# Performance work log

Hardware: AMD Instinct MI355X
Metric: run time of the kernel (lower is better)

The kernel has to match this reference:

```python
import jax, jax.numpy as jnp
import numpy as np
from jax import lax

WIN = 9
PAD = WIN // 2


def _box_sum(x):
    # x: [B,1,H,W]; all-ones WINxWIN conv, stride 1, pad PAD -> same spatial size
    k = jnp.ones((1, 1, WIN, WIN), dtype=x.dtype)
    return lax.conv_general_dilated(
        x, k, window_strides=(1, 1), padding=[(PAD, PAD), (PAD, PAD)],
        dimension_numbers=("NCHW", "OIHW", "NCHW"))


def setup_inputs() -> dict:
    key = jax.random.key(0)
    k1, k2 = jax.random.split(key)
    B, C, H, W = 32, 1, 512, 512
    y_true = jax.random.uniform(k1, (B, C, H, W), dtype=jnp.float32)
    y_pred = jax.random.uniform(k2, (B, C, H, W), dtype=jnp.float32)
    return {"y_true": y_true, "y_pred": y_pred}


def reference(y_true, y_pred):
    Ii, Ji = y_true, y_pred
    win_size = float(WIN * WIN)
    I_sum = _box_sum(Ii)
    J_sum = _box_sum(Ji)
    I2_sum = _box_sum(Ii * Ii)
    J2_sum = _box_sum(Ji * Ji)
    IJ_sum = _box_sum(Ii * Ji)
    u_I = I_sum / win_size
    u_J = J_sum / win_size
    cross = IJ_sum - u_J * I_sum - u_I * J_sum + u_I * u_J * win_size
    I_var = I2_sum - 2.0 * u_I * I_sum + u_I * u_I * win_size
    J_var = J2_sum - 2.0 * u_J * J_sum + u_J * u_J * win_size
    cc = cross * cross / (I_var * J_var + 1e-05)
    return -jnp.mean(cc)
```

## Files before the change

kernel.cpp:

```cpp
#include <hip/hip_runtime.h>


#define BATCH   32
#define IMH     512
#define IMW     512
#define SH      16
#define NSTRIP  32
#define NPART   (BATCH * NSTRIP)
#define VROW    520
#define NK      (SH + 8)

#define HWIN(QI, HA, HB) do {                                              \
    const float2 w0_ = *(const float2*)&Vbuf[QI][c0];                      \
    const float2 w1_ = *(const float2*)&Vbuf[QI][c0 + 2];                  \
    const float2 w2_ = *(const float2*)&Vbuf[QI][c0 + 4];                  \
    const float2 w3_ = *(const float2*)&Vbuf[QI][c0 + 6];                  \
    const float2 w4_ = *(const float2*)&Vbuf[QI][c0 + 8];                  \
    HA = ((w0_.x + w0_.y) + (w1_.x + w1_.y))                               \
       + ((w2_.x + w2_.y) + (w3_.x + w3_.y)) + w4_.x;                      \
    HB = HA + w4_.y - w0_.x;                                               \
} while (0)

#define CC1(AI, AJ, S2, S3, S4) do {                                       \
    const float cross = (S4) - (AI)*(AJ)*inv81;                            \
    const float ivv   = (S2) - (AI)*(AI)*inv81;                            \
    const float jvv   = (S3) - (AJ)*(AJ)*inv81;                            \
    acc += cross * cross * __builtin_amdgcn_rcpf(ivv * jvv + 1e-5f);       \
} while (0)

__global__ __launch_bounds__(256, 4) void ncc_main(const float* __restrict__ I,
                                                   const float* __restrict__ J,
                                                   float* __restrict__ partial) {
    const int u  = threadIdx.x;
    const int s  = blockIdx.x;
    const int b  = blockIdx.y;
    const int r0 = s * SH;
    const int c0 = 2 * u;
    const float inv81 = 1.0f / 81.0f;

    const float* Ib = I + (size_t)b * IMH * IMW;
    const float* Jb = J + (size_t)b * IMH * IMW;

    __shared__ float  Vbuf[5][VROW];
    __shared__ float4 ring[9][256];

    if (u < 40) {
        const int q = u >> 3, p = u & 7;
        Vbuf[q][p < 4 ? p : 512 + p] = 0.f;
    }
    __syncthreads();

    float VI0 = 0.f, VI1 = 0.f, VJ0 = 0.f, VJ1 = 0.f;
    float VII0 = 0.f, VII1 = 0.f, VJJ0 = 0.f, VJJ1 = 0.f;
    float VIJ0 = 0.f, VIJ1 = 0.f;
    float acc = 0.f;
    int slot = 0;

    float2 ai = make_float2(0.f, 0.f), aj = make_float2(0.f, 0.f);
    {
        const int ri = r0 - 4;
        if ((unsigned)ri < (unsigned)IMH) {
            ai = *(const float2*)(Ib + (size_t)ri * IMW + c0);
            aj = *(const float2*)(Jb + (size_t)ri * IMW + c0);
        }
    }

#pragma unroll 1
    for (int K = 0; K < NK; ++K) {
        float2 nai = make_float2(0.f, 0.f), naj = make_float2(0.f, 0.f);
        {
            const int rin = r0 - 3 + K;
            if (K + 1 < NK && (unsigned)rin < (unsigned)IMH) {
                nai = *(const float2*)(Ib + (size_t)rin * IMW + c0);
                naj = *(const float2*)(Jb + (size_t)rin * IMW + c0);
            }
        }

        float4 oldv = make_float4(0.f, 0.f, 0.f, 0.f);
        if (K >= 9) oldv = ring[slot][u];
        ring[slot][u] = make_float4(ai.x, ai.y, aj.x, aj.y);
        slot = (slot == 8) ? 0 : slot + 1;

        VI0  += ai.x - oldv.x;             VI1  += ai.y - oldv.y;
        VJ0  += aj.x - oldv.z;             VJ1  += aj.y - oldv.w;
        VII0 += ai.x*ai.x - oldv.x*oldv.x; VII1 += ai.y*ai.y - oldv.y*oldv.y;
        VJJ0 += aj.x*aj.x - oldv.z*oldv.z; VJJ1 += aj.y*aj.y - oldv.w*oldv.w;
        VIJ0 += ai.x*aj.x - oldv.x*oldv.z; VIJ1 += ai.y*aj.y - oldv.y*oldv.w;

        if (K >= 8) {
            *(float2*)&Vbuf[0][4 + c0] = make_float2(VI0,  VI1);
            *(float2*)&Vbuf[1][4 + c0] = make_float2(VJ0,  VJ1);
            *(float2*)&Vbuf[2][4 + c0] = make_float2(VII0, VII1);
            *(float2*)&Vbuf[3][4 + c0] = make_float2(VJJ0, VJJ1);
            *(float2*)&Vbuf[4][4 + c0] = make_float2(VIJ0, VIJ1);
            __syncthreads();
            float HI0, HI1, HJ0, HJ1, HA0, HA1, HB0, HB1, HC0, HC1;
            HWIN(0, HI0, HI1);
            HWIN(1, HJ0, HJ1);
            HWIN(2, HA0, HA1);
            HWIN(3, HB0, HB1);
            HWIN(4, HC0, HC1);
            CC1(HI0, HJ0, HA0, HB0, HC0);
            CC1(HI1, HJ1, HA1, HB1, HC1);
            __syncthreads();
        }

        ai = nai; aj = naj;
    }

    float sum = acc;
#pragma unroll
    for (int off = 32; off > 0; off >>= 1) sum += __shfl_down(sum, off, 64);

    __shared__ float wsum[4];
    if ((u & 63) == 0) wsum[u >> 6] = sum;
    __syncthreads();
    if (u == 0) {
        partial[(size_t)b * NSTRIP + s] = wsum[0] + wsum[1] + wsum[2] + wsum[3];
    }
}

__global__ __launch_bounds__(256) void ncc_reduce(const float* __restrict__ partial,
                                                  float* __restrict__ out) {
    const int t = threadIdx.x;
    double ssum = 0.0;
    for (int idx = t; idx < NPART; idx += 256) ssum += (double)partial[idx];
#pragma unroll
    for (int off = 32; off > 0; off >>= 1) ssum += __shfl_down(ssum, off, 64);

    __shared__ double wsum[4];
    if ((t & 63) == 0) wsum[t >> 6] = ssum;
    __syncthreads();
    if (t == 0) {
        const double total = wsum[0] + wsum[1] + wsum[2] + wsum[3];
        out[0] = (float)(-total / 8388608.0);
    }
}

extern "C" void kernel_launch(void* const* d_in, const int* in_sizes, int n_in,
                              void* d_out, int out_size, void* d_ws, size_t ws_size,
                              hipStream_t stream) {
    const float* I = (const float*)d_in[0];
    const float* J = (const float*)d_in[1];
    float* partial = (float*)d_ws;
    float* out     = (float*)d_out;

    dim3 grid(NSTRIP, BATCH);
    ncc_main<<<grid, 256, 0, stream>>>(I, J, partial);
    ncc_reduce<<<1, 256, 0, stream>>>(partial, out);
}
```

Measured before the change: 118.4 us.

## Split image rows into 128-column wavefront blocks with halo columns

Each 256-thread block handling a full 512-wide row strip is replaced by four 64-thread single-wavefront blocks, each covering 128 columns. Every block computes vertical sums for 8 extra halo columns, kept in a separate ring and written into a smaller shared buffer. The intent is cheaper barriers within one wavefront, a shorter cross-wave reduction, and more, smaller blocks for scheduling. In exchange, halo columns add redundant loads and vertical-sum work, and the halo loads and updates are done by only 8 lanes, which causes divergence.

```diff
diff --git a/kernel.cpp b/kernel.cpp
--- a/kernel.cpp
+++ b/kernel.cpp
@@ -1,21 +1,38 @@
 #include <hip/hip_runtime.h>
 
 
-#define BATCH   32
-#define IMH     512
-#define IMW     512
-#define SH      16
-#define NSTRIP  32
-#define NPART   (BATCH * NSTRIP)
-#define VROW    520
-#define NK      (SH + 8)
+#define BATCH     32
+#define IMH       512
+#define IMW       512
+#define SH        16
+#define NROWSTRIP 32
+#define NCOLSTRIP 4
+#define CBW       128
+#define NPART     (BATCH * NROWSTRIP * NCOLSTRIP)
+#define NK        (SH + 8)
+#define VROW      136
+
+#define LOADROW(RI, CI, CJ, HI, HJ) do {                                   \
+    const int ri_ = (RI);                                                  \
+    CI = make_float2(0.f, 0.f); CJ = make_float2(0.f, 0.f);                \
+    HI = 0.f; HJ = 0.f;                                                    \
+    if ((unsigned)ri_ < (unsigned)IMH) {                                   \
+        const float* rI_ = Ib + (size_t)ri_ * IMW;                         \
+        const float* rJ_ = Jb + (size_t)ri_ * IMW;                         \
+        CI = *(const float2*)(rI_ + cc0);                                  \
+        CJ = *(const float2*)(rJ_ + cc0);                                  \
+        if (u < 8 && (unsigned)hc < (unsigned)IMW) {                       \
+            HI = rI_[hc]; HJ = rJ_[hc];                                    \
+        }                                                                  \
+    }                                                                      \
+} while (0)
 
 #define HWIN(QI, HA, HB) do {                                              \
-    const float2 w0_ = *(const float2*)&Vbuf[QI][c0];                      \
-    const float2 w1_ = *(const float2*)&Vbuf[QI][c0 + 2];                  \
-    const float2 w2_ = *(const float2*)&Vbuf[QI][c0 + 4];                  \
-    const float2 w3_ = *(const float2*)&Vbuf[QI][c0 + 6];                  \
-    const float2 w4_ = *(const float2*)&Vbuf[QI][c0 + 8];                  \
+    const float2 w0_ = *(const float2*)&Vbuf[QI][l0];                      \
+    const float2 w1_ = *(const float2*)&Vbuf[QI][l0 + 2];                  \
+    const float2 w2_ = *(const float2*)&Vbuf[QI][l0 + 4];                  \
+    const float2 w3_ = *(const float2*)&Vbuf[QI][l0 + 6];                  \
+    const float2 w4_ = *(const float2*)&Vbuf[QI][l0 + 8];                  \
     HA = ((w0_.x + w0_.y) + (w1_.x + w1_.y))                               \
        + ((w2_.x + w2_.y) + (w3_.x + w3_.y)) + w4_.x;                      \
     HB = HA + w4_.y - w0_.x;                                               \
@@ -28,71 +45,73 @@
     acc += cross * cross * __builtin_amdgcn_rcpf(ivv * jvv + 1e-5f);       \
 } while (0)
 
-__global__ __launch_bounds__(256, 4) void ncc_main(const float* __restrict__ I,
-                                                   const float* __restrict__ J,
-                                                   float* __restrict__ partial) {
-    const int u  = threadIdx.x;
-    const int s  = blockIdx.x;
-    const int b  = blockIdx.y;
-    const int r0 = s * SH;
-    const int c0 = 2 * u;
+__global__ __launch_bounds__(64) void ncc_main(const float* __restrict__ I,
+                                               const float* __restrict__ J,
+                                               float* __restrict__ partial) {
+    const int u    = threadIdx.x;
+    const int cs   = blockIdx.x;
+    const int s    = blockIdx.y;
+    const int b    = blockIdx.z;
+    const int r0   = s * SH;
+    const int cblk = cs * CBW;
+    const int cc0  = cblk + 2 * u;
+    const int hc   = cblk + (u < 4 ? u - 4 : 124 + u);
+    const int hx   = (u < 4) ? u : 128 + u;
+    const int l0   = 2 * u;
     const float inv81 = 1.0f / 81.0f;
 
     const float* Ib = I + (size_t)b * IMH * IMW;
     const float* Jb = J + (size_t)b * IMH * IMW;
 
+    __shared__ float4 ring[9][64];
+    __shared__ float2 ringH[9][8];
     __shared__ float  Vbuf[5][VROW];
-    __shared__ float4 ring[9][256];
-
-    if (u < 40) {
-        const int q = u >> 3, p = u & 7;
-        Vbuf[q][p < 4 ? p : 512 + p] = 0.f;
-    }
-    __syncthreads();
 
     float VI0 = 0.f, VI1 = 0.f, VJ0 = 0.f, VJ1 = 0.f;
     float VII0 = 0.f, VII1 = 0.f, VJJ0 = 0.f, VJJ1 = 0.f;
     float VIJ0 = 0.f, VIJ1 = 0.f;
+    float hVI = 0.f, hVJ = 0.f, hVII = 0.f, hVJJ = 0.f, hVIJ = 0.f;
     float acc = 0.f;
     int slot = 0;
 
-    float2 ai = make_float2(0.f, 0.f), aj = make_float2(0.f, 0.f);
-    {
-        const int ri = r0 - 4;
-        if ((unsigned)ri < (unsigned)IMH) {
-            ai = *(const float2*)(Ib + (size_t)ri * IMW + c0);
-            aj = *(const float2*)(Jb + (size_t)ri * IMW + c0);
-        }
-    }
+    float2 ci, cj; float hi, hj;
+    LOADROW(r0 - 4, ci, cj, hi, hj);
 
 #pragma unroll 1
     for (int K = 0; K < NK; ++K) {
-        float2 nai = make_float2(0.f, 0.f), naj = make_float2(0.f, 0.f);
-        {
-            const int rin = r0 - 3 + K;
-            if (K + 1 < NK && (unsigned)rin < (unsigned)IMH) {
-                nai = *(const float2*)(Ib + (size_t)rin * IMW + c0);
-                naj = *(const float2*)(Jb + (size_t)rin * IMW + c0);
-            }
-        }
+        float2 ni, nj; float nhi, nhj;
+        LOADROW((K + 1 < NK) ? (r0 - 3 + K) : -1, ni, nj, nhi, nhj);
 
         float4 oldv = make_float4(0.f, 0.f, 0.f, 0.f);
-        if (K >= 9) oldv = ring[slot][u];
-        ring[slot][u] = make_float4(ai.x, ai.y, aj.x, aj.y);
+        float2 oldh = make_float2(0.f, 0.f);
+        if (K >= 9) {
+            oldv = ring[slot][u];
+            if (u < 8) oldh = ringH[slot][u];
+        }
+        ring[slot][u] = make_float4(ci.x, ci.y, cj.x, cj.y);
+        if (u < 8) ringH[slot][u] = make_float2(hi, hj);
         slot = (slot == 8) ? 0 : slot + 1;
 
-        VI0  += ai.x - oldv.x;             VI1  += ai.y - oldv.y;
-        VJ0  += aj.x - oldv.z;             VJ1  += aj.y - oldv.w;
-        VII0 += ai.x*ai.x - oldv.x*oldv.x; VII1 += ai.y*ai.y - oldv.y*oldv.y;
-        VJJ0 += aj.x*aj.x - oldv.z*oldv.z; VJJ1 += aj.y*aj.y - oldv.w*oldv.w;
-        VIJ0 += ai.x*aj.x - oldv.x*oldv.z; VIJ1 += ai.y*aj.y - oldv.y*oldv.w;
+        VI0  += ci.x - oldv.x;             VI1  += ci.y - oldv.y;
+        VJ0  += cj.x - oldv.z;             VJ1  += cj.y - oldv.w;
+        VII0 += ci.x*ci.x - oldv.x*oldv.x; VII1 += ci.y*ci.y - oldv.y*oldv.y;
+        VJJ0 += cj.x*cj.x - oldv.z*oldv.z; VJJ1 += cj.y*cj.y - oldv.w*oldv.w;
+        VIJ0 += ci.x*cj.x - oldv.x*oldv.z; VIJ1 += ci.y*cj.y - oldv.y*oldv.w;
+        hVI  += hi - oldh.x;               hVJ  += hj - oldh.y;
+        hVII += hi*hi - oldh.x*oldh.x;
+        hVJJ += hj*hj - oldh.y*oldh.y;
+        hVIJ += hi*hj - oldh.x*oldh.y;
 
         if (K >= 8) {
-            *(float2*)&Vbuf[0][4 + c0] = make_float2(VI0,  VI1);
-            *(float2*)&Vbuf[1][4 + c0] = make_float2(VJ0,  VJ1);
-            *(float2*)&Vbuf[2][4 + c0] = make_float2(VII0, VII1);
-            *(float2*)&Vbuf[3][4 + c0] = make_float2(VJJ0, VJJ1);
-            *(float2*)&Vbuf[4][4 + c0] = make_float2(VIJ0, VIJ1);
+            *(float2*)&Vbuf[0][4 + l0] = make_float2(VI0,  VI1);
+            *(float2*)&Vbuf[1][4 + l0] = make_float2(VJ0,  VJ1);
+            *(float2*)&Vbuf[2][4 + l0] = make_float2(VII0, VII1);
+            *(float2*)&Vbuf[3][4 + l0] = make_float2(VJJ0, VJJ1);
+            *(float2*)&Vbuf[4][4 + l0] = make_float2(VIJ0, VIJ1);
+            if (u < 8) {
+                Vbuf[0][hx] = hVI;  Vbuf[1][hx] = hVJ;  Vbuf[2][hx] = hVII;
+                Vbuf[3][hx] = hVJJ; Vbuf[4][hx] = hVIJ;
+            }
             __syncthreads();
             float HI0, HI1, HJ0, HJ1, HA0, HA1, HB0, HB1, HC0, HC1;
             HWIN(0, HI0, HI1);
@@ -105,18 +124,14 @@
             __syncthreads();
         }
 
-        ai = nai; aj = naj;
+        ci = ni; cj = nj; hi = nhi; hj = nhj;
     }
 
     float sum = acc;
 #pragma unroll
     for (int off = 32; off > 0; off >>= 1) sum += __shfl_down(sum, off, 64);
-
-    __shared__ float wsum[4];
-    if ((u & 63) == 0) wsum[u >> 6] = sum;
-    __syncthreads();
     if (u == 0) {
-        partial[(size_t)b * NSTRIP + s] = wsum[0] + wsum[1] + wsum[2] + wsum[3];
+        partial[((size_t)b * NROWSTRIP + s) * NCOLSTRIP + cs] = sum;
     }
 }
 
@@ -145,7 +160,7 @@
     float* partial = (float*)d_ws;
     float* out     = (float*)d_out;
 
-    dim3 grid(NSTRIP, BATCH);
-    ncc_main<<<grid, 256, 0, stream>>>(I, J, partial);
+    dim3 grid(NCOLSTRIP, NROWSTRIP, BATCH);
+    ncc_main<<<grid, 64, 0, stream>>>(I, J, partial);
     ncc_reduce<<<1, 256, 0, stream>>>(partial, out);
 }
```

Result: slower. 126.8 us (+7.0%).

## Fully unroll row loop with register ring buffer and 4-deep prefetch

Applied to the files above, without the earlier changes.

Replaces the shared-memory float4 ring buffer of the last 9 input rows with 18 named float2 registers. The row loop is fully unrolled so register indices are static, and global loads are now issued four rows ahead instead of one. This removes LDS traffic for the ring and hides more global-memory latency, at the cost of higher register pressure under launch_bounds(256,4) and larger code size.

```diff
diff --git a/kernel.cpp b/kernel.cpp
--- a/kernel.cpp
+++ b/kernel.cpp
@@ -7,8 +7,17 @@
 #define SH      16
 #define NSTRIP  32
 #define NPART   (BATCH * NSTRIP)
+#define NK      24
 #define VROW    520
-#define NK      (SH + 8)
+
+#define PREF(K, PI, PJ) do {                                               \
+    const int ri_ = r0 - 4 + (K);                                          \
+    PI = make_float2(0.f, 0.f); PJ = make_float2(0.f, 0.f);                \
+    if ((unsigned)ri_ < (unsigned)IMH) {                                   \
+        PI = *(const float2*)(Ib + (size_t)ri_ * IMW + c0);                \
+        PJ = *(const float2*)(Jb + (size_t)ri_ * IMW + c0);                \
+    }                                                                      \
+} while (0)
 
 #define HWIN(QI, HA, HB) do {                                              \
     const float2 w0_ = *(const float2*)&Vbuf[QI][c0];                      \
@@ -28,94 +37,110 @@
     acc += cross * cross * __builtin_amdgcn_rcpf(ivv * jvv + 1e-5f);       \
 } while (0)
 
+#define EMIT() do {                                                        \
+    *(float2*)&Vbuf[0][4 + c0] = make_float2(VI0, VI1);                    \
+    *(float2*)&Vbuf[1][4 + c0] = make_float2(VJ0, VJ1);                    \
+    *(float2*)&Vbuf[2][4 + c0] = make_float2(VA0, VA1);                    \
+    *(float2*)&Vbuf[3][4 + c0] = make_float2(VB0, VB1);                    \
+    *(float2*)&Vbuf[4][4 + c0] = make_float2(VC0, VC1);                    \
+    __syncthreads();                                                       \
+    float HI0, HI1, HJ0, HJ1, HA0, HA1, HB0, HB1, HC0, HC1;                \
+    HWIN(0, HI0, HI1);                                                     \
+    HWIN(1, HJ0, HJ1);                                                     \
+    HWIN(2, HA0, HA1);                                                     \
+    HWIN(3, HB0, HB1);                                                     \
+    HWIN(4, HC0, HC1);                                                     \
+    CC1(HI0, HJ0, HA0, HB0, HC0);                                          \
+    CC1(HI1, HJ1, HA1, HB1, HC1);                                          \
+    __syncthreads();           \
+} while (0)
+
+#define STEP(K, PI, PJ, RI_, RJ_) do {                                     \
+    if ((K) >= 9) {                                                        \
+        VI0 -= RI_.x;        VI1 -= RI_.y;                                 \
+        VJ0 -= RJ_.x;        VJ1 -= RJ_.y;                                 \
+        VA0 -= RI_.x*RI_.x;  VA1 -= RI_.y*RI_.y;                           \
+        VB0 -= RJ_.x*RJ_.x;  VB1 -= RJ_.y*RJ_.y;                           \
+        VC0 -= RI_.x*RJ_.x;  VC1 -= RI_.y*RJ_.y;                           \
+    }                                                                      \
+    VI0 += PI.x;        VI1 += PI.y;                                       \
+    VJ0 += PJ.x;        VJ1 += PJ.y;                                       \
+    VA0 += PI.x*PI.x;   VA1 += PI.y*PI.y;                                  \
+    VB0 += PJ.x*PJ.x;   VB1 += PJ.y*PJ.y;                                  \
+    VC0 += PI.x*PJ.x;   VC1 += PI.y*PJ.y;                                  \
+    RI_ = PI; RJ_ = PJ;                                                    \
+    if ((K) >= 8) { EMIT(); }                                              \
+} while (0)
+
 __global__ __launch_bounds__(256, 4) void ncc_main(const float* __restrict__ I,
                                                    const float* __restrict__ J,
                                                    float* __restrict__ partial) {
-    const int u  = threadIdx.x;
+    const int t  = threadIdx.x;
     const int s  = blockIdx.x;
     const int b  = blockIdx.y;
     const int r0 = s * SH;
-    const int c0 = 2 * u;
+    const int c0 = 2 * t;
     const float inv81 = 1.0f / 81.0f;
 
     const float* Ib = I + (size_t)b * IMH * IMW;
     const float* Jb = J + (size_t)b * IMH * IMW;
 
-    __shared__ float  Vbuf[5][VROW];
-    __shared__ float4 ring[9][256];
-
-    if (u < 40) {
-        const int q = u >> 3, p = u & 7;
+    __shared__ float Vbuf[5][VROW];
+    if (t < 40) {
+        const int q = t >> 3, p = t & 7;
         Vbuf[q][p < 4 ? p : 512 + p] = 0.f;
     }
     __syncthreads();
 
+    const float2 z_ = make_float2(0.f, 0.f);
+    float2 rIA = z_, rIB = z_, rIC = z_, rID = z_, rIE = z_,
+           rIF = z_, rIG = z_, rIH = z_, rII = z_;
+    float2 rJA = z_, rJB = z_, rJC = z_, rJD = z_, rJE = z_,
+           rJF = z_, rJG = z_, rJH = z_, rJI = z_;
     float VI0 = 0.f, VI1 = 0.f, VJ0 = 0.f, VJ1 = 0.f;
-    float VII0 = 0.f, VII1 = 0.f, VJJ0 = 0.f, VJJ1 = 0.f;
-    float VIJ0 = 0.f, VIJ1 = 0.f;
+    float VA0 = 0.f, VA1 = 0.f, VB0 = 0.f, VB1 = 0.f;
+    float VC0 = 0.f, VC1 = 0.f;
     float acc = 0.f;
-    int slot = 0;
+    float2 pi0, pj0, pi1, pj1, pi2, pj2, pi3, pj3;
 
-    float2 ai = make_float2(0.f, 0.f), aj = make_float2(0.f, 0.f);
-    {
-        const int ri = r0 - 4;
-        if ((unsigned)ri < (unsigned)IMH) {
-            ai = *(const float2*)(Ib + (size_t)ri * IMW + c0);
-            aj = *(const float2*)(Jb + (size_t)ri * IMW + c0);
-        }
-    }
+    PREF(0, pi0, pj0);
+    PREF(1, pi1, pj1);
+    PREF(2, pi2, pj2);
+    PREF(3, pi3, pj3);
 
-#pragma unroll 1
-    for (int K = 0; K < NK; ++K) {
-        float2 nai = make_float2(0.f, 0.f), naj = make_float2(0.f, 0.f);
-        {
-            const int rin = r0 - 3 + K;
-            if (K + 1 < NK && (unsigned)rin < (unsigned)IMH) {
-                nai = *(const float2*)(Ib + (size_t)rin * IMW + c0);
-                naj = *(const float2*)(Jb + (size_t)rin * IMW + c0);
-            }
-        }
-
-        float4 oldv = make_float4(0.f, 0.f, 0.f, 0.f);
-        if (K >= 9) oldv = ring[slot][u];
-        ring[slot][u] = make_float4(ai.x, ai.y, aj.x, aj.y);
-        slot = (slot == 8) ? 0 : slot + 1;
-
-        VI0  += ai.x - oldv.x;             VI1  += ai.y - oldv.y;
-        VJ0  += aj.x - oldv.z;             VJ1  += aj.y - oldv.w;
-        VII0 += ai.x*ai.x - oldv.x*oldv.x; VII1 += ai.y*ai.y - oldv.y*oldv.y;
-        VJJ0 += aj.x*aj.x - oldv.z*oldv.z; VJJ1 += aj.y*aj.y - oldv.w*oldv.w;
-        VIJ0 += ai.x*aj.x - oldv.x*oldv.z; VIJ1 += ai.y*aj.y - oldv.y*oldv.w;
-
-        if (K >= 8) {
-            *(float2*)&Vbuf[0][4 + c0] = make_float2(VI0,  VI1);
-            *(float2*)&Vbuf[1][4 + c0] = make_float2(VJ0,  VJ1);
-            *(float2*)&Vbuf[2][4 + c0] = make_float2(VII0, VII1);
-            *(float2*)&Vbuf[3][4 + c0] = make_float2(VJJ0, VJJ1);
-            *(float2*)&Vbuf[4][4 + c0] = make_float2(VIJ0, VIJ1);
-            __syncthreads();
-            float HI0, HI1, HJ0, HJ1, HA0, HA1, HB0, HB1, HC0, HC1;
-            HWIN(0, HI0, HI1);
-            HWIN(1, HJ0, HJ1);
-            HWIN(2, HA0, HA1);
-            HWIN(3, HB0, HB1);
-            HWIN(4, HC0, HC1);
-            CC1(HI0, HJ0, HA0, HB0, HC0);
-            CC1(HI1, HJ1, HA1, HB1, HC1);
-            __syncthreads();
-        }
-
-        ai = nai; aj = naj;
-    }
+    STEP( 0, pi0, pj0, rIA, rJA);  PREF( 4, pi0, pj0);
+    STEP( 1, pi1, pj1, rIB, rJB);  PREF( 5, pi1, pj1);
+    STEP( 2, pi2, pj2, rIC, rJC);  PREF( 6, pi2, pj2);
+    STEP( 3, pi3, pj3, rID, rJD);  PREF( 7, pi3, pj3);
+    STEP( 4, pi0, pj0, rIE, rJE);  PREF( 8, pi0, pj0);
+    STEP( 5, pi1, pj1, rIF, rJF);  PREF( 9, pi1, pj1);
+    STEP( 6, pi2, pj2, rIG, rJG);  PREF(10, pi2, pj2);
+    STEP( 7, pi3, pj3, rIH, rJH);  PREF(11, pi3, pj3);
+    STEP( 8, pi0, pj0, rII, rJI);  PREF(12, pi0, pj0);
+    STEP( 9, pi1, pj1, rIA, rJA);  PREF(13, pi1, pj1);
+    STEP(10, pi2, pj2, rIB, rJB);  PREF(14, pi2, pj2);
+    STEP(11, pi3, pj3, rIC, rJC);  PREF(15, pi3, pj3);
+    STEP(12, pi0, pj0, rID, rJD);  PREF(16, pi0, pj0);
+    STEP(13, pi1, pj1, rIE, rJE);  PREF(17, pi1, pj1);
+    STEP(14, pi2, pj2, rIF, rJF);  PREF(18, pi2, pj2);
+    STEP(15, pi3, pj3, rIG, rJG);  PREF(19, pi3, pj3);
+    STEP(16, pi0, pj0, rIH, rJH);  PREF(20, pi0, pj0);
+    STEP(17, pi1, pj1, rII, rJI);  PREF(21, pi1, pj1);
+    STEP(18, pi2, pj2, rIA, rJA);  PREF(22, pi2, pj2);
+    STEP(19, pi3, pj3, rIB, rJB);  PREF(23, pi3, pj3);
+    STEP(20, pi0, pj0, rIC, rJC);
+    STEP(21, pi1, pj1, rID, rJD);
+    STEP(22, pi2, pj2, rIE, rJE);
+    STEP(23, pi3, pj3, rIF, rJF);
 
     float sum = acc;
 #pragma unroll
     for (int off = 32; off > 0; off >>= 1) sum += __shfl_down(sum, off, 64);
 
     __shared__ float wsum[4];
-    if ((u & 63) == 0) wsum[u >> 6] = sum;
+    if ((t & 63) == 0) wsum[t >> 6] = sum;
     __syncthreads();
-    if (u == 0) {
+    if (t == 0) {
         partial[(size_t)b * NSTRIP + s] = wsum[0] + wsum[1] + wsum[2] + wsum[3];
     }
 }
```

Measured after the change: 232.5 us. +96.3%, slower.
